# Kernel optimization log

Measured on AMD Instinct MI355X. Metric: run time of the kernel, lower is better.

Reference implementation:

```python
import jax, jax.numpy as jnp
import numpy as np

N_HEADS = 16
N_KV_HEADS = 8
DIM = 2048
HEAD_DIM = DIM // N_HEADS  # 128
N_REP = N_HEADS // N_KV_HEADS


def _rope(t, cos, sin):
    # t: [B, S, H, D]; cos/sin: [S, D//2]
    t2 = t.reshape(*t.shape[:-1], -1, 2)  # [B,S,H,D/2,2]
    p1, p2 = t2[..., 0], t2[..., 1]
    c = cos[None, :, None, :]
    s = sin[None, :, None, :]
    r1 = p1 * c - p2 * s
    r2 = p1 * s + p2 * c
    return jnp.stack((r1, r2), axis=-1).reshape(t.shape)


def setup_inputs() -> dict:
    key = jax.random.key(0)
    ks = jax.random.split(key, 7)
    B, S = 2, 2048
    x = jax.random.normal(ks[0], (B, S, DIM), dtype=jnp.float32)
    freqs_cos = jax.random.normal(ks[1], (S, HEAD_DIM // 2), dtype=jnp.float32)
    freqs_sin = jax.random.normal(ks[2], (S, HEAD_DIM // 2), dtype=jnp.float32)
    sc = 1.0 / np.sqrt(DIM)
    wq = jax.random.normal(ks[3], (DIM, N_HEADS * HEAD_DIM), dtype=jnp.float32) * sc
    wk = jax.random.normal(ks[4], (DIM, N_KV_HEADS * HEAD_DIM), dtype=jnp.float32) * sc
    wv = jax.random.normal(ks[5], (DIM, N_KV_HEADS * HEAD_DIM), dtype=jnp.float32) * sc
    wo = jax.random.normal(ks[6], (N_HEADS * HEAD_DIM, DIM), dtype=jnp.float32) * sc
    return {"x": x, "freqs_cos": freqs_cos, "freqs_sin": freqs_sin,
            "wq": wq, "wk": wk, "wv": wv, "wo": wo}


def reference(x, freqs_cos, freqs_sin, wq, wk, wv, wo):
    B, S, _ = x.shape
    xq = (x @ wq).reshape(B, S, N_HEADS, HEAD_DIM)
    xk = (x @ wk).reshape(B, S, N_KV_HEADS, HEAD_DIM)
    xv = (x @ wv).reshape(B, S, N_KV_HEADS, HEAD_DIM)
    xq = _rope(xq, freqs_cos, freqs_sin)
    xk = _rope(xk, freqs_cos, freqs_sin)
    # GQA repeat_kv: [B,S,Hkv,D] -> [B,S,Hkv*n_rep,D]
    xk = jnp.repeat(xk, N_REP, axis=2)
    xv = jnp.repeat(xv, N_REP, axis=2)
    q = xq.transpose(0, 2, 1, 3)  # [B,H,S,D]
    k = xk.transpose(0, 2, 1, 3)
    v = xv.transpose(0, 2, 1, 3)
    scale = 1.0 / np.sqrt(HEAD_DIM)
    scores = jnp.einsum('bhqd,bhkd->bhqk', q, k) * scale
    causal = jnp.tril(jnp.ones((S, S), dtype=bool))
    scores = jnp.where(causal[None, None], scores, -jnp.inf)
    probs = jax.nn.softmax(scores.astype(jnp.float32), axis=-1).astype(q.dtype)
    out = jnp.einsum('bhqk,bhkd->bhqd', probs, v)
    out = out.transpose(0, 2, 1, 3).reshape(B, S, N_HEADS * HEAD_DIM)
    return out @ wo
```

## Files before the change

### kernel.cpp

```cpp
#include <hip/hip_runtime.h>
#include <cstdint>
#include <cstddef>

#define S_LEN 2048
#define DIM_   2048
#define NH   16
#define NKV  8
#define HD   128

typedef __attribute__((ext_vector_type(8))) __bf16 bf16x8;
typedef __attribute__((ext_vector_type(4))) float  f32x4;

typedef const __attribute__((address_space(1))) void* gptr_t;
typedef __attribute__((address_space(3))) void*       sptr_t;

static __device__ __forceinline__ float bf2f(unsigned short u) {
  union { unsigned int i; float f; } v; v.i = ((unsigned int)u) << 16; return v.f;
}
static __device__ __forceinline__ unsigned short f2bf(float f) {
  union { float f; unsigned int i; } v; v.f = f;
  unsigned int u = v.i;
  unsigned int r = (u + 0x7FFFu + ((u >> 16) & 1u)) >> 16;
  return (unsigned short)r;
}

#define QSCALE 0.12751744f
#define RESC_THR 11.542f

__global__ void k_prep(const float* __restrict__ x, unsigned short* __restrict__ xb,
                       const float* __restrict__ wq, const float* __restrict__ wk,
                       const float* __restrict__ wv, const float* __restrict__ wo,
                       unsigned short* __restrict__ wqkvT, unsigned short* __restrict__ woT) {
  int bid = blockIdx.x;
  if (bid < 8192) {
    int i = bid * 256 + threadIdx.x;
    float4 v = ((const float4*)x)[i];
    ushort4 o; o.x = f2bf(v.x); o.y = f2bf(v.y); o.z = f2bf(v.z); o.w = f2bf(v.w);
    ((ushort4*)xb)[i] = o;
    return;
  }
  bid -= 8192;
  const float* src; unsigned short* dst; int N, ntx;
  if (bid < 4096)      { src = wq; dst = wqkvT;                       N = 2048; ntx = 64; }
  else if (bid < 6144) { bid -= 4096; src = wk; dst = wqkvT + (size_t)2048 * 2048; N = 1024; ntx = 32; }
  else if (bid < 8192) { bid -= 6144; src = wv; dst = wqkvT + (size_t)3072 * 2048; N = 1024; ntx = 32; }
  else                 { bid -= 8192; src = wo; dst = woT;            N = 2048; ntx = 64; }
  const int K = 2048;
  __shared__ float tile[32][33];
  int lx = threadIdx.x & 31, ly = threadIdx.x >> 5;
  int r0 = (bid / ntx) * 32, c0 = (bid % ntx) * 32;
  #pragma unroll
  for (int r = 0; r < 32; r += 8)
    tile[ly + r][lx] = src[(size_t)(r0 + ly + r) * N + c0 + lx];
  __syncthreads();
  #pragma unroll
  for (int r = 0; r < 32; r += 8)
    dst[(size_t)(c0 + ly + r) * K + r0 + lx] = f2bf(tile[lx][ly + r]);
}

template<int MODE>
__global__ __launch_bounds__(256, 2) void k_gemm_bt(
    const unsigned short* __restrict__ A, const unsigned short* __restrict__ BT,
    void* __restrict__ C, int N, int K,
    const float* __restrict__ fc, const float* __restrict__ fs,
    unsigned short* __restrict__ kb, unsigned short* __restrict__ vb) {
  __shared__ __align__(16) unsigned short Asm[128 * 64];
  __shared__ __align__(16) unsigned short Bsm[128 * 64];
  const int t = threadIdx.x;
  const int lane = t & 63, w = t >> 6;
  const int wm = (w >> 1) * 64, wn = (w & 1) * 64;
  const int col = lane & 15, quad = lane >> 4;
  const int m0 = blockIdx.y * 128, n0 = blockIdx.x * 128;

  f32x4 acc[4][4];
  #pragma unroll
  for (int i = 0; i < 4; i++)
    #pragma unroll
    for (int j = 0; j < 4; j++) acc[i][j] = (f32x4){0.f, 0.f, 0.f, 0.f};

  for (int kk = 0; kk < K; kk += 64) {
    #pragma unroll
    for (int r = 0; r < 4; ++r) {
      int c = t + r * 256;
      int c0 = (t & ~63) + r * 256;
      int row = c >> 3;
      int kcs = (c & 7) ^ (row & 7);
      const unsigned short* gA = A + (size_t)(m0 + row) * K + kk + kcs * 8;
      const unsigned short* gB = BT + (size_t)(n0 + row) * K + kk + kcs * 8;
      __builtin_amdgcn_global_load_lds((gptr_t)gA, (sptr_t)(&Asm[c0 * 8]), 16, 0, 0);
      __builtin_amdgcn_global_load_lds((gptr_t)gB, (sptr_t)(&Bsm[c0 * 8]), 16, 0, 0);
    }
    __syncthreads();
    #pragma unroll
    for (int kc2 = 0; kc2 < 2; kc2++) {
      bf16x8 af[4], bf[4];
      #pragma unroll
      for (int mi = 0; mi < 4; mi++) {
        int rowA = wm + mi * 16 + col;
        af[mi] = *(const bf16x8*)(&Asm[rowA * 64 + (((kc2 * 4 + quad) ^ (col & 7)) * 8)]);
      }
      #pragma unroll
      for (int ni = 0; ni < 4; ni++) {
        int rowB = wn + ni * 16 + col;
        bf[ni] = *(const bf16x8*)(&Bsm[rowB * 64 + (((kc2 * 4 + quad) ^ (col & 7)) * 8)]);
      }
      #pragma unroll
      for (int mi = 0; mi < 4; mi++)
        #pragma unroll
        for (int ni = 0; ni < 4; ni++)
          acc[mi][ni] = __builtin_amdgcn_mfma_f32_16x16x32_bf16(af[mi], bf[ni], acc[mi][ni], 0, 0, 0);
    }
    __syncthreads();
  }

  #pragma unroll
  for (int mi = 0; mi < 4; mi++) {
    int row_base = m0 + wm + mi * 16 + quad * 4;
    #pragma unroll
    for (int ni = 0; ni < 4; ni++) {
      int col_g = n0 + wn + ni * 16 + col;
      if (MODE == 1) {
        float* O = (float*)C;
        #pragma unroll
        for (int r = 0; r < 4; r++) O[(size_t)(row_base + r) * N + col_g] = acc[mi][ni][r];
      } else {
        int region = col_g >> 10;
        if (region < 3) {
          int ri = (col_g & 127) >> 1;
          float sgn = (col_g & 1) ? 1.f : -1.f;
          unsigned short* qO = (unsigned short*)C;
          #pragma unroll
          for (int r = 0; r < 4; r++) {
            int row = row_base + r;
            int s = row & (S_LEN - 1);
            float cv = fc[s * 64 + ri], sv = fs[s * 64 + ri];
            float val = acc[mi][ni][r];
            float other = __shfl_xor(val, 1);
            float res = val * cv + sgn * other * sv;
            if (region < 2) qO[(size_t)row * 2048 + col_g] = f2bf(res * QSCALE);
            else            kb[(size_t)row * 1024 + (col_g - 2048)] = f2bf(res);
          }
        } else {
          int n_local = col_g - 3072;
          int b = row_base >> 11, s = row_base & (S_LEN - 1);
          int kvh = n_local >> 7, d = n_local & (HD - 1);
          ushort4 o4;
          o4.x = f2bf(acc[mi][ni][0]); o4.y = f2bf(acc[mi][ni][1]);
          o4.z = f2bf(acc[mi][ni][2]); o4.w = f2bf(acc[mi][ni][3]);
          *(ushort4*)(&vb[((size_t)((b * NKV + kvh) * HD + d)) * S_LEN + s]) = o4;
        }
      }
    }
  }
}

#define KLD 136
#define VLD 72
__global__ __launch_bounds__(512, 3) void k_attn(
    const unsigned short* __restrict__ q, const unsigned short* __restrict__ k,
    const unsigned short* __restrict__ vT, unsigned short* __restrict__ ao) {
  __shared__ __align__(16) unsigned short Ksm[64 * KLD];
  __shared__ __align__(16) unsigned short Vsm[128 * VLD];
  __shared__ __align__(16) unsigned short Psm[8 * 16 * VLD];
  const int t = threadIdx.x;
  const int lane = t & 63, w = t >> 6;
  const int col = lane & 15, quad = lane >> 4;
  const int g = blockIdx.x;
  const int b = g >> 3, kvh = g & 7;
  const int h = kvh * 2 + (w >> 2);
  const int yi = blockIdx.y;
  const int my_qt = (yi < 16) ? yi : 47 - yi;
  const int qrow = my_qt * 64 + (w & 3) * 16;
  unsigned short* Pw = &Psm[w * 16 * VLD];

  bf16x8 qf[4];
  const size_t qbase = ((size_t)(b * S_LEN) + qrow + col) * DIM_ + h * HD;
  #pragma unroll
  for (int kc = 0; kc < 4; kc++) qf[kc] = *(const bf16x8*)(q + qbase + kc * 32 + quad * 8);

  f32x4 o[8];
  #pragma unroll
  for (int i = 0; i < 8; i++) o[i] = (f32x4){0.f, 0.f, 0.f, 0.f};
  float m_i[4] = {-1e30f, -1e30f, -1e30f, -1e30f};
  float l_i[4] = {0.f, 0.f, 0.f, 0.f};

  const int nkt = my_qt + 1;
  for (int kt = 0; kt < nkt; ++kt) {
    #pragma unroll
    for (int cc = 0; cc < 2; cc++) {
      int c = t + cc * 512;
      int i = c >> 4, dc = c & 15;
      *(uint4*)(&Ksm[i * KLD + dc * 8]) =
          *(const uint4*)(k + ((size_t)(b * S_LEN + kt * 64 + i)) * (NKV * HD) + kvh * HD + dc * 8);
    }
    #pragma unroll
    for (int cc = 0; cc < 2; cc++) {
      int c = t + cc * 512;
      int d = c >> 3, kc2 = c & 7;
      *(uint4*)(&Vsm[d * VLD + kc2 * 8]) =
          *(const uint4*)(vT + ((size_t)((b * NKV + kvh) * HD + d)) * S_LEN + kt * 64 + kc2 * 8);
    }
    __syncthreads();

    float p[4][4];
    __builtin_amdgcn_s_setprio(1);
    #pragma unroll
    for (int nt = 0; nt < 4; nt++) {
      f32x4 s_acc = (f32x4){0.f, 0.f, 0.f, 0.f};
      #pragma unroll
      for (int kc = 0; kc < 4; kc++) {
        bf16x8 kf = *(const bf16x8*)(&Ksm[(nt * 16 + col) * KLD + kc * 32 + quad * 8]);
        s_acc = __builtin_amdgcn_mfma_f32_16x16x32_bf16(qf[kc], kf, s_acc, 0, 0, 0);
      }
      #pragma unroll
      for (int r = 0; r < 4; r++) p[nt][r] = s_acc[r];
    }
    __builtin_amdgcn_s_setprio(0);
    if (kt == my_qt) {
      #pragma unroll
      for (int nt = 0; nt < 4; nt++) {
        int key = kt * 64 + nt * 16 + col;
        #pragma unroll
        for (int r = 0; r < 4; r++) {
          int rg = qrow + quad * 4 + r;
          if (key > rg) p[nt][r] = -1e30f;
        }
      }
    }
    float mnew[4];
    float need = -1e30f;
    #pragma unroll
    for (int r = 0; r < 4; r++) {
      float mx = fmaxf(fmaxf(p[0][r], p[1][r]), fmaxf(p[2][r], p[3][r]));
      mx = fmaxf(mx, __shfl_xor(mx, 1));
      mx = fmaxf(mx, __shfl_xor(mx, 2));
      mx = fmaxf(mx, __shfl_xor(mx, 4));
      mx = fmaxf(mx, __shfl_xor(mx, 8));
      mnew[r] = mx;
      need = fmaxf(need, mx - m_i[r]);
    }
    if (__any(need > RESC_THR)) {
      #pragma unroll
      for (int r = 0; r < 4; r++) {
        float mn = fmaxf(m_i[r], mnew[r]);
        float alpha = exp2f(m_i[r] - mn);
        m_i[r] = mn;
        l_i[r] *= alpha;
        #pragma unroll
        for (int dt = 0; dt < 8; dt++) o[dt][r] *= alpha;
      }
    }
    float rsum[4] = {0.f, 0.f, 0.f, 0.f};
    #pragma unroll
    for (int nt = 0; nt < 4; nt++)
      #pragma unroll
      for (int r = 0; r < 4; r++) {
        float e = exp2f(p[nt][r] - m_i[r]);
        p[nt][r] = e;
        rsum[r] += e;
      }
    #pragma unroll
    for (int r = 0; r < 4; r++) {
      float rs = rsum[r];
      rs += __shfl_xor(rs, 1);
      rs += __shfl_xor(rs, 2);
      rs += __shfl_xor(rs, 4);
      rs += __shfl_xor(rs, 8);
      l_i[r] += rs;
    }

    #pragma unroll
    for (int nt = 0; nt < 4; nt++)
      #pragma unroll
      for (int r = 0; r < 4; r++)
        Pw[(quad * 4 + r) * VLD + nt * 16 + col] = f2bf(p[nt][r]);
    asm volatile("s_waitcnt lgkmcnt(0)" ::: "memory");
    bf16x8 pf[2];
    #pragma unroll
    for (int kc2 = 0; kc2 < 2; kc2++)
      pf[kc2] = *(const bf16x8*)(&Pw[col * VLD + kc2 * 32 + quad * 8]);

    __builtin_amdgcn_s_setprio(1);
    #pragma unroll
    for (int dt = 0; dt < 8; dt++) {
      #pragma unroll
      for (int kc2 = 0; kc2 < 2; kc2++) {
        bf16x8 vf = *(const bf16x8*)(&Vsm[(dt * 16 + col) * VLD + kc2 * 32 + quad * 8]);
        o[dt] = __builtin_amdgcn_mfma_f32_16x16x32_bf16(pf[kc2], vf, o[dt], 0, 0, 0);
      }
    }
    __builtin_amdgcn_s_setprio(0);
    __syncthreads();
  }

  #pragma unroll
  for (int dt = 0; dt < 8; dt++) {
    int dcol = h * HD + dt * 16 + col;
    #pragma unroll
    for (int r = 0; r < 4; r++) {
      int rg = qrow + quad * 4 + r;
      ao[((size_t)(b * S_LEN) + rg) * DIM_ + dcol] = f2bf(o[dt][r] / l_i[r]);
    }
  }
}

extern "C" void kernel_launch(void* const* d_in, const int* in_sizes, int n_in,
                              void* d_out, int out_size, void* d_ws, size_t ws_size,
                              hipStream_t stream) {
  const float* x  = (const float*)d_in[0];
  const float* fc = (const float*)d_in[1];
  const float* fs = (const float*)d_in[2];
  const float* wq = (const float*)d_in[3];
  const float* wk = (const float*)d_in[4];
  const float* wv = (const float*)d_in[5];
  const float* wo = (const float*)d_in[6];
  float* out = (float*)d_out;

  char* ws = (char*)d_ws;
  const size_t MB = 1024 * 1024;
  unsigned short* xb    = (unsigned short*)(ws + 0 * MB);
  unsigned short* wqkvT = (unsigned short*)(ws + 16 * MB);
  unsigned short* woT   = (unsigned short*)(ws + 32 * MB);
  unsigned short* qb    = (unsigned short*)(ws + 40 * MB);
  unsigned short* kb    = (unsigned short*)(ws + 56 * MB);
  unsigned short* vT    = (unsigned short*)(ws + 64 * MB);
  unsigned short* ao    = (unsigned short*)(ws + 72 * MB);

  k_prep<<<dim3(20480), dim3(256), 0, stream>>>(x, xb, wq, wk, wv, wo, wqkvT, woT);
  k_gemm_bt<3><<<dim3(32, 32), dim3(256), 0, stream>>>(xb, wqkvT, (void*)qb, 4096, 2048, fc, fs, kb, vT);
  k_attn<<<dim3(16, 32), dim3(512), 0, stream>>>(qb, kb, vT, ao);
  k_gemm_bt<1><<<dim3(16, 32), dim3(256), 0, stream>>>(ao, woT, (void*)out, 2048, 2048, nullptr, nullptr, nullptr, nullptr);
}
```

Measured before the change: 348.0 us.

## Prefetch next K/V tiles into registers and transpose QK MFMA for per-lane softmax

The attention loop now loads the next K and V tiles into registers while the current tile is being computed, and stores them to shared memory at points split by barriers. This hides global load latency behind the MFMA and softmax work. The QK^T MFMA operands are swapped so each lane holds one query column. That reduces the row max and sum to two cross-quad shuffles, keeps a single m/l scalar per lane, and lets P be written as packed 64-bit stores. Launch bounds drop from 3 to 2 waves per EU to make room for the extra prefetch registers, which may lower occupancy.

```diff
diff --git a/kernel.cpp b/kernel.cpp
--- a/kernel.cpp
+++ b/kernel.cpp
@@ -156,7 +156,7 @@
 
 #define KLD 136
 #define VLD 72
-__global__ __launch_bounds__(512, 3) void k_attn(
+__global__ __launch_bounds__(512, 2) void k_attn(
     const unsigned short* __restrict__ q, const unsigned short* __restrict__ k,
     const unsigned short* __restrict__ vT, unsigned short* __restrict__ ao) {
   __shared__ __align__(16) unsigned short Ksm[64 * KLD];
@@ -173,6 +173,13 @@
   const int qrow = my_qt * 64 + (w & 3) * 16;
   unsigned short* Pw = &Psm[w * 16 * VLD];
 
+  const int ki0 = t >> 4,        kdc = t & 15;
+  const int ki1 = (t + 512) >> 4;
+  const int vd0 = t >> 3,        vkc = t & 7;
+  const int vd1 = (t + 512) >> 3;
+  const unsigned short* kgp = k + (size_t)(b * S_LEN) * (NKV * HD) + kvh * HD + kdc * 8;
+  const unsigned short* vgp = vT + ((size_t)(b * NKV + kvh) * HD) * S_LEN + vkc * 8;
+
   bf16x8 qf[4];
   const size_t qbase = ((size_t)(b * S_LEN) + qrow + col) * DIM_ + h * HD;
   #pragma unroll
@@ -181,26 +188,30 @@
   f32x4 o[8];
   #pragma unroll
   for (int i = 0; i < 8; i++) o[i] = (f32x4){0.f, 0.f, 0.f, 0.f};
-  float m_i[4] = {-1e30f, -1e30f, -1e30f, -1e30f};
-  float l_i[4] = {0.f, 0.f, 0.f, 0.f};
+  float m_i = -1e30f;
+  float l_i = 0.f;
 
   const int nkt = my_qt + 1;
+
+  {
+    uint4 kr0 = *(const uint4*)(kgp + (size_t)ki0 * (NKV * HD));
+    uint4 kr1 = *(const uint4*)(kgp + (size_t)ki1 * (NKV * HD));
+    uint4 vr0 = *(const uint4*)(vgp + (size_t)vd0 * S_LEN);
+    uint4 vr1 = *(const uint4*)(vgp + (size_t)vd1 * S_LEN);
+    *(uint4*)(&Ksm[ki0 * KLD + kdc * 8]) = kr0;
+    *(uint4*)(&Ksm[ki1 * KLD + kdc * 8]) = kr1;
+    *(uint4*)(&Vsm[vd0 * VLD + vkc * 8]) = vr0;
+    *(uint4*)(&Vsm[vd1 * VLD + vkc * 8]) = vr1;
+  }
+  __syncthreads();
+
   for (int kt = 0; kt < nkt; ++kt) {
-    #pragma unroll
-    for (int cc = 0; cc < 2; cc++) {
-      int c = t + cc * 512;
-      int i = c >> 4, dc = c & 15;
-      *(uint4*)(&Ksm[i * KLD + dc * 8]) =
-          *(const uint4*)(k + ((size_t)(b * S_LEN + kt * 64 + i)) * (NKV * HD) + kvh * HD + dc * 8);
-    }
-    #pragma unroll
-    for (int cc = 0; cc < 2; cc++) {
-      int c = t + cc * 512;
-      int d = c >> 3, kc2 = c & 7;
-      *(uint4*)(&Vsm[d * VLD + kc2 * 8]) =
-          *(const uint4*)(vT + ((size_t)((b * NKV + kvh) * HD + d)) * S_LEN + kt * 64 + kc2 * 8);
-    }
-    __syncthreads();
+    const bool more = (kt + 1 < nkt);
+    uint4 kr0, kr1, vr0, vr1;
+    if (more) {
+      kr0 = *(const uint4*)(kgp + (size_t)((kt + 1) * 64 + ki0) * (NKV * HD));
+      kr1 = *(const uint4*)(kgp + (size_t)((kt + 1) * 64 + ki1) * (NKV * HD));
+    }
 
     float p[4][4];
     __builtin_amdgcn_s_setprio(1);
@@ -210,71 +221,70 @@
       #pragma unroll
       for (int kc = 0; kc < 4; kc++) {
         bf16x8 kf = *(const bf16x8*)(&Ksm[(nt * 16 + col) * KLD + kc * 32 + quad * 8]);
-        s_acc = __builtin_amdgcn_mfma_f32_16x16x32_bf16(qf[kc], kf, s_acc, 0, 0, 0);
+        s_acc = __builtin_amdgcn_mfma_f32_16x16x32_bf16(kf, qf[kc], s_acc, 0, 0, 0);
       }
       #pragma unroll
       for (int r = 0; r < 4; r++) p[nt][r] = s_acc[r];
     }
     __builtin_amdgcn_s_setprio(0);
+
     if (kt == my_qt) {
-      #pragma unroll
-      for (int nt = 0; nt < 4; nt++) {
-        int key = kt * 64 + nt * 16 + col;
+      const int qglob = qrow + col;
+      #pragma unroll
+      for (int nt = 0; nt < 4; nt++)
         #pragma unroll
-        for (int r = 0; r < 4; r++) {
-          int rg = qrow + quad * 4 + r;
-          if (key > rg) p[nt][r] = -1e30f;
-        }
-      }
-    }
-    float mnew[4];
-    float need = -1e30f;
-    #pragma unroll
-    for (int r = 0; r < 4; r++) {
-      float mx = fmaxf(fmaxf(p[0][r], p[1][r]), fmaxf(p[2][r], p[3][r]));
-      mx = fmaxf(mx, __shfl_xor(mx, 1));
-      mx = fmaxf(mx, __shfl_xor(mx, 2));
-      mx = fmaxf(mx, __shfl_xor(mx, 4));
-      mx = fmaxf(mx, __shfl_xor(mx, 8));
-      mnew[r] = mx;
-      need = fmaxf(need, mx - m_i[r]);
-    }
-    if (__any(need > RESC_THR)) {
+        for (int r = 0; r < 4; r++)
+          if (kt * 64 + nt * 16 + quad * 4 + r > qglob) p[nt][r] = -1e30f;
+    }
+
+    float mx = fmaxf(fmaxf(fmaxf(p[0][0], p[0][1]), fmaxf(p[0][2], p[0][3])),
+                     fmaxf(fmaxf(p[1][0], p[1][1]), fmaxf(p[1][2], p[1][3])));
+    mx = fmaxf(mx, fmaxf(fmaxf(fmaxf(p[2][0], p[2][1]), fmaxf(p[2][2], p[2][3])),
+                         fmaxf(fmaxf(p[3][0], p[3][1]), fmaxf(p[3][2], p[3][3]))));
+    mx = fmaxf(mx, __shfl_xor(mx, 16));
+    mx = fmaxf(mx, __shfl_xor(mx, 32));
+    if (__any(mx - m_i > RESC_THR)) {
+      float mn = fmaxf(m_i, mx);
+      float alpha = exp2f(m_i - mn);
+      m_i = mn; l_i *= alpha;
+      float ar[4];
+      #pragma unroll
+      for (int r = 0; r < 4; r++) ar[r] = __shfl(alpha, quad * 4 + r);
+      #pragma unroll
+      for (int dt = 0; dt < 8; dt++)
+        #pragma unroll
+        for (int r = 0; r < 4; r++) o[dt][r] *= ar[r];
+    }
+    float rs = 0.f;
+    #pragma unroll
+    for (int nt = 0; nt < 4; nt++)
       #pragma unroll
       for (int r = 0; r < 4; r++) {
-        float mn = fmaxf(m_i[r], mnew[r]);
-        float alpha = exp2f(m_i[r] - mn);
-        m_i[r] = mn;
-        l_i[r] *= alpha;
-        #pragma unroll
-        for (int dt = 0; dt < 8; dt++) o[dt][r] *= alpha;
-      }
-    }
-    float rsum[4] = {0.f, 0.f, 0.f, 0.f};
-    #pragma unroll
-    for (int nt = 0; nt < 4; nt++)
-      #pragma unroll
-      for (int r = 0; r < 4; r++) {
-        float e = exp2f(p[nt][r] - m_i[r]);
+        float e = exp2f(p[nt][r] - m_i);
         p[nt][r] = e;
-        rsum[r] += e;
-      }
-    #pragma unroll
-    for (int r = 0; r < 4; r++) {
-      float rs = rsum[r];
-      rs += __shfl_xor(rs, 1);
-      rs += __shfl_xor(rs, 2);
-      rs += __shfl_xor(rs, 4);
-      rs += __shfl_xor(rs, 8);
-      l_i[r] += rs;
-    }
-
-    #pragma unroll
-    for (int nt = 0; nt < 4; nt++)
-      #pragma unroll
-      for (int r = 0; r < 4; r++)
-        Pw[(quad * 4 + r) * VLD + nt * 16 + col] = f2bf(p[nt][r]);
-    asm volatile("s_waitcnt lgkmcnt(0)" ::: "memory");
+        rs += e;
+      }
+    rs += __shfl_xor(rs, 16);
+    rs += __shfl_xor(rs, 32);
+    l_i += rs;
+
+    #pragma unroll
+    for (int nt = 0; nt < 4; nt++) {
+      unsigned int w0 = (unsigned int)f2bf(p[nt][0]) | ((unsigned int)f2bf(p[nt][1]) << 16);
+      unsigned int w1 = (unsigned int)f2bf(p[nt][2]) | ((unsigned int)f2bf(p[nt][3]) << 16);
+      uint2 pk; pk.x = w0; pk.y = w1;
+      *(uint2*)(&Pw[col * VLD + nt * 16 + quad * 4]) = pk;
+    }
+
+    __syncthreads();
+
+    if (more) {
+      *(uint4*)(&Ksm[ki0 * KLD + kdc * 8]) = kr0;
+      *(uint4*)(&Ksm[ki1 * KLD + kdc * 8]) = kr1;
+      vr0 = *(const uint4*)(vgp + (size_t)vd0 * S_LEN + (kt + 1) * 64);
+      vr1 = *(const uint4*)(vgp + (size_t)vd1 * S_LEN + (kt + 1) * 64);
+    }
+
     bf16x8 pf[2];
     #pragma unroll
     for (int kc2 = 0; kc2 < 2; kc2++)
@@ -290,16 +300,25 @@
       }
     }
     __builtin_amdgcn_s_setprio(0);
+
     __syncthreads();
-  }
-
+
+    if (more) {
+      *(uint4*)(&Vsm[vd0 * VLD + vkc * 8]) = vr0;
+      *(uint4*)(&Vsm[vd1 * VLD + vkc * 8]) = vr1;
+    }
+  }
+
+  float linv[4];
+  #pragma unroll
+  for (int r = 0; r < 4; r++) linv[r] = 1.f / __shfl(l_i, quad * 4 + r);
   #pragma unroll
   for (int dt = 0; dt < 8; dt++) {
     int dcol = h * HD + dt * 16 + col;
     #pragma unroll
     for (int r = 0; r < 4; r++) {
       int rg = qrow + quad * 4 + r;
-      ao[((size_t)(b * S_LEN) + rg) * DIM_ + dcol] = f2bf(o[dt][r] / l_i[r]);
+      ao[((size_t)(b * S_LEN) + rg) * DIM_ + dcol] = f2bf(o[dt][r] * linv[r]);
     }
   }
 }
```

Result: faster. 335.9 us (-3.5%).
